# Optimization experiments

Hardware: AMD Instinct MI355X
Metric: run time of the kernel (lower is better)

Reference implementation:

```python
import jax, jax.numpy as jnp
import numpy as np

EPS = 1e-4  # ReEig eigenvalue clamp threshold (standard SPDNet value)


def _eig_apply(X, fn):
    # symmetric eig, apply fn to eigenvalues, reconstruct: V diag(fn(w)) V^T
    w, v = jnp.linalg.eigh(X)
    return jnp.einsum('...ij,...j,...kj->...ik', v, fn(w), v)


def _congr(P, G, mode):
    # CongrG: G^{+/-1/2} P G^{+/-1/2}, G is a single [n,n] SPD matrix
    w, v = jnp.linalg.eigh(G)
    s = jnp.sqrt(w) if mode == 'pos' else 1.0 / jnp.sqrt(w)
    Gs = (v * s) @ v.T  # [n,n]
    return Gs @ P @ Gs


def setup_inputs() -> dict:
    key = jax.random.key(0)
    ks = jax.random.split(key, 8)
    B, win, band, n, h, n_mid = 512, 3, 9, 22, 27, 32
    # SPD input covariance-like matrices
    M = jax.random.normal(ks[0], (B, win, band, n, n), dtype=jnp.float32)
    x = M @ jnp.swapaxes(M, -1, -2) / n + 0.5 * jnp.eye(n, dtype=jnp.float32)
    # Stiefel BiMap weights (orthonormal columns)
    W1, _ = jnp.linalg.qr(jax.random.normal(ks[1], (h, n_mid, n_mid), dtype=jnp.float32))
    Q2, _ = jnp.linalg.qr(jax.random.normal(ks[2], (h, n_mid, n_mid), dtype=jnp.float32))
    W2 = Q2[..., :n]
    running_mean = jnp.eye(n, dtype=jnp.float32)
    Aw = jax.random.normal(ks[3], (n, n), dtype=jnp.float32)
    bn_weight = Aw @ Aw.T / n + jnp.eye(n, dtype=jnp.float32)
    conv_w = jax.random.normal(ks[4], (48, 1, win, band * n * n), dtype=jnp.float32) * 0.01
    conv_b = jnp.zeros((48,), dtype=jnp.float32)
    fc_w = jax.random.normal(ks[5], (4, 48), dtype=jnp.float32) * 0.1
    fc_b = jnp.zeros((4,), dtype=jnp.float32)
    return {"x": x, "W1": W1, "W2": W2, "running_mean": running_mean,
            "bn_weight": bn_weight, "conv_w": conv_w, "conv_b": conv_b,
            "fc_w": fc_w, "fc_b": fc_b}


def reference(x, W1, W2, running_mean, bn_weight, conv_w, conv_b, fc_w, fc_b):
    B, win, band, n, _ = x.shape
    h = win * band
    no1 = W1.shape[-1]
    X = x.reshape(B, h, n, n)
    # SPDIncreaseDim(n -> no1): E X E^T + diag([0]*n + [1]*(no1-n))
    pad = no1 - n
    X = jnp.pad(X, ((0, 0), (0, 0), (0, pad), (0, pad)))
    X = X + jnp.diag(jnp.concatenate([jnp.zeros(n), jnp.ones(pad)])).astype(x.dtype)
    # BiMap 1 (per-channel W^T X W) + ReEig
    P = jnp.einsum('hni,bhnm,hmj->bhij', W1, X, W1)
    P = _eig_apply(P, lambda w: jnp.maximum(w, EPS))
    # BiMap 2
    P = jnp.einsum('hni,bhnm,hmj->bhij', W2, P, W2)
    # BatchNormSPD (eval mode): center by running_mean, scale by weight
    P = _congr(P, running_mean, 'neg')
    P = _congr(P, bn_weight, 'pos')
    # ReEig + LogEig
    P = _eig_apply(P, lambda w: jnp.maximum(w, EPS))
    P = _eig_apply(P, jnp.log)
    x_vec = P.reshape(B, win, band * n * n)
    feat = jnp.einsum('bhw,chw->bc', x_vec, conv_w[:, 0]) + conv_b  # [B, 48]
    return feat @ fc_w.T + fc_b                       # [B, classes]
```

## Files before the change

kernel.cpp:

```cpp
#include <hip/hip_runtime.h>


#define WS_CONST 484
#define WS_VT    512
#define WS_V     (512 + 13068)
#define WS_D     (13580 + 14256)
#define WS_G     (27836 + 13068)
#define G_STRIDE 528
#define V_STRIDE 528

typedef float v2f __attribute__((ext_vector_type(2)));

static __device__ __forceinline__ float dpp_shl1(float x) {
  return __int_as_float(__builtin_amdgcn_mov_dpp(__float_as_int(x), 0x101, 0xf, 0xf, true));
}
static __device__ __forceinline__ float upd_shr1(float old, float x) {
  return __int_as_float(__builtin_amdgcn_update_dpp(
      __float_as_int(old), __float_as_int(x), 0x111, 0xf, 0xf, false));
}

static __device__ __forceinline__ void rot_cs(float nL, float nR, float d,
                                              float& c, float& s,
                                              float& c2, float& ss, float& cs2) {
  float mu   = 0.5f*(nR - nL);
  float r2   = __builtin_fmaf(mu, mu, d*d);
  float invr = __builtin_amdgcn_rsqf(r2);
  bool  degen = (r2 < 1e-40f);
  float co = fminf(fabsf(mu)*invr, 1.0f);
  co = degen ? 1.0f : co;
  c2 = __builtin_fmaf(0.5f, co, 0.5f);
  c  = sqrtf(c2);
  float cinv = __builtin_amdgcn_rcpf(c);
  float t2 = d*invr;
  t2 = (mu < 0.0f) ? -t2 : t2;
  cs2 = degen ? 0.0f : t2;
  s  = 0.5f*cs2*cinv;
  ss = 1.0f - c2;
}

static __device__ __forceinline__ void jacobi_sweeps(v2f wl[11], v2f wr[11],
                                                     bool act, bool inert,
                                                     int minsweep, float eps2) {
  int okprev = 0;
  #pragma unroll 1
  for (int sweep = 0; sweep < 5; ++sweep) {
    if (sweep >= minsweep && __all(okprev)) break;
    v2f na = (v2f)(0.f), nb = (v2f)(0.f);
    #pragma unroll
    for (int i = 0; i < 11; ++i) { na += wl[i]*wl[i]; nb += wr[i]*wr[i]; }
    float nL = na.x + na.y, nR = nb.x + nb.y;
    float q = inert ? 0.f : (nL*nL + nR*nR);
    q += __shfl_xor(q, 1, 16);
    q += __shfl_xor(q, 2, 16);
    q += __shfl_xor(q, 4, 16);
    q += __shfl_xor(q, 8, 16);
    float dacc = 0.f;
    #pragma unroll 1
    for (int r = 0; r < 11; ++r) {
      {
        v2f da = (v2f)(0.f), db = (v2f)(0.f);
        #pragma unroll
        for (int i = 0; i < 10; i += 2) { da += wl[i]*wr[i]; db += wl[i+1]*wr[i+1]; }
        da += wl[10]*wr[10];
        float d = (da.x + da.y) + (db.x + db.y);
        dacc += d*d;
        float c, s, c2, ss, cs2;
        rot_cs(nL, nR, d, c, s, c2, ss, cs2);
        float nLn = c2*nL - cs2*d + ss*nR;
        float nRn = ss*nL + cs2*d + c2*nR;
        v2f cv = (v2f)(c), sv = (v2f)(s);
        #pragma unroll
        for (int i = 0; i < 11; ++i) {
          v2f nl = cv*wl[i] - sv*wr[i];
          v2f nr = sv*wl[i] + cv*wr[i];
          wl[i] = nr;
          wr[i] = nl;
        }
        nL = nRn; nR = nLn;
      }
      {
        v2f u[11];
        #pragma unroll
        for (int i = 0; i < 11; ++i) { u[i].x = dpp_shl1(wl[i].x); u[i].y = dpp_shl1(wl[i].y); }
        float nU = dpp_shl1(nL);
        v2f da = (v2f)(0.f), db = (v2f)(0.f);
        #pragma unroll
        for (int i = 0; i < 10; i += 2) { da += wr[i]*u[i]; db += wr[i+1]*u[i+1]; }
        da += wr[10]*u[10];
        float d = (da.x + da.y) + (db.x + db.y);
        d = act ? d : 0.f;
        dacc += d*d;
        float c, s, c2, ss, cs2;
        rot_cs(nR, nU, d, c, s, c2, ss, cs2);
        v2f cv = (v2f)(c), sv = (v2f)(s);
        #pragma unroll
        for (int i = 0; i < 11; ++i) {
          v2f rl = cv*wr[i] - sv*u[i];
          v2f rr = sv*wr[i] + cv*u[i];
          wr[i].x = act ? rr.x : wr[i].x;
          wr[i].y = act ? rr.y : wr[i].y;
          wl[i].x = upd_shr1(wl[i].x, rl.x);
          wl[i].y = upd_shr1(wl[i].y, rl.y);
        }
        float nRn = ss*nR + cs2*d + c2*nU;
        float nLg = c2*nR - cs2*d + ss*nU;
        nR = act ? nRn : nR;
        nL = upd_shr1(nL, nLg);
      }
    }
    float ds = inert ? 0.f : dacc;
    ds += __shfl_xor(ds, 1, 16);
    ds += __shfl_xor(ds, 2, 16);
    ds += __shfl_xor(ds, 4, 16);
    ds += __shfl_xor(ds, 8, 16);
    okprev = (ds <= eps2*q);
  }
}

__global__ void prep_kernel(const float* __restrict__ rm, const float* __restrict__ bn,
                            const float* __restrict__ W1, const float* __restrict__ W2,
                            const float* __restrict__ conv_w, const float* __restrict__ fc_w,
                            const float* __restrict__ conv_b, const float* __restrict__ fc_b,
                            float* __restrict__ ws, float* __restrict__ out) {
  __shared__ float sW1[1024] __attribute__((aligned(16)));
  __shared__ float sW2[704]  __attribute__((aligned(16)));
  __shared__ float sY[2][2][484] __attribute__((aligned(16)));
  __shared__ float sZ[2][2][484] __attribute__((aligned(16)));
  __shared__ float sT[2][484]    __attribute__((aligned(16)));
  __shared__ float sS[484]  __attribute__((aligned(16)));
  __shared__ float sU[704]  __attribute__((aligned(16)));
  __shared__ float sE[220]  __attribute__((aligned(16)));
  __shared__ float sG[1936] __attribute__((aligned(16)));
  __shared__ float sC[2];
  const int tid = threadIdx.x, h = blockIdx.x;

  if (h == 0)
    for (int idx = tid; idx < 2048; idx += 256) out[idx] = 0.f;

  const int wv = tid >> 6, ln = tid & 63;
  if (wv < 2) {
    const float* src = wv ? rm : bn;
    float s = 0.f;
    for (int i = ln; i < 484; i += 64) { float v = src[i]; s += v*v; }
    s += __shfl_xor(s, 1);  s += __shfl_xor(s, 2);  s += __shfl_xor(s, 4);
    s += __shfl_xor(s, 8);  s += __shfl_xor(s, 16); s += __shfl_xor(s, 32);
    if (ln == 0) sC[wv] = sqrtf(s);
  } else {
    const int t = tid - 128;
    for (int i = t; i < 1024; i += 128) sW1[i] = W1[h*1024 + i];
    for (int i = t; i < 704;  i += 128) sW2[i] = W2[h*704 + i];
  }
  __syncthreads();

  {
    const float ic0 = 1.0f/sC[0], ic1 = 1.0f/sC[1];
    for (int idx = tid; idx < 484; idx += 256) {
      const int i = idx/22, j = idx - 22*i;
      const float e = (i == j) ? 1.f : 0.f;
      sY[0][0][idx] = bn[idx]*ic0;  sZ[0][0][idx] = e;
      sY[1][0][idx] = rm[idx]*ic1;  sZ[1][0][idx] = e;
    }
  }
  __syncthreads();

  int cur = 0;
  #pragma unroll 1
  for (int it = 0; it < 11; ++it) {
    for (int idx = tid; idx < 484; idx += 256) {
      const int mt = (idx >= 242), r = idx - mt*242, i = r/11, jp = r - 11*i;
      const float* Zc = sZ[mt][cur];
      const float* Yc = sY[mt][cur];
      v2f acc = (v2f)(0.f);
      #pragma unroll
      for (int k = 0; k < 22; ++k)
        acc += *(const v2f*)(Yc + k*22 + 2*jp) * Zc[i*22 + k];
      v2f tv;
      tv.x = ((2*jp     == i) ? 3.f : 0.f) - acc.x;
      tv.y = ((2*jp + 1 == i) ? 3.f : 0.f) - acc.y;
      *(v2f*)(sT[mt] + i*22 + 2*jp) = tv;
    }
    __syncthreads();
    for (int idx = tid; idx < 968; idx += 256) {
      const int sel = idx/242, r = idx - 242*sel, i = r/11, jp = r - 11*i;
      const int mt = sel >> 1; const bool isZ = sel & 1;
      const float* A = isZ ? sT[mt] : sY[mt][cur];
      const float* B = isZ ? sZ[mt][cur] : sT[mt];
      v2f acc = (v2f)(0.f);
      #pragma unroll
      for (int k = 0; k < 22; ++k)
        acc += *(const v2f*)(B + k*22 + 2*jp) * A[i*22 + k];
      *(v2f*)((isZ ? sZ[mt][cur^1] : sY[mt][cur^1]) + i*22 + 2*jp) = 0.5f*acc;
    }
    __syncthreads();
    cur ^= 1;
  }

  {
    const float scale = sqrtf(sC[0]/sC[1]);
    const float* Zrm = sZ[1][cur];
    const float* Ybn = sY[0][cur];
    for (int idx = tid; idx < 484; idx += 256) {
      const int i = idx/22, j = idx - 22*i;
      float s = 0.f;
      for (int k = 0; k < 22; ++k) s += Zrm[i*22+k]*Ybn[k*22+j];
      sS[idx] = scale*s;
    }
  }
  for (int idx = tid; idx < 704; idx += 256) {
    const int n = idx/22, j = idx - 22*n;
    float s = 0.f;
    for (int k = 0; k < 32; ++k) s += sW1[n*32+k]*sW2[k*22+j];
    sU[idx] = s;
  }
  if (tid < 242) {
    const int wi = h/9, bi = h - 9*wi;
    const float* base = conv_w + wi*4356 + bi*484 + 2*tid;
    v2f a0 = (v2f)(0.f), a1 = (v2f)(0.f), a2 = (v2f)(0.f), a3 = (v2f)(0.f);
    #pragma unroll
    for (int c = 0; c < 48; ++c) {
      const v2f wv2 = *(const v2f*)(base + c*13068);
      a0 += wv2*fc_w[c];
      a1 += wv2*fc_w[48+c];
      a2 += wv2*fc_w[96+c];
      a3 += wv2*fc_w[144+c];
    }
    *(v2f*)(sG +        2*tid) = a0;
    *(v2f*)(sG +  484 + 2*tid) = a1;
    *(v2f*)(sG +  968 + 2*tid) = a2;
    *(v2f*)(sG + 1452 + 2*tid) = a3;
  }
  __syncthreads();

  for (int idx = tid; idx < 484; idx += 256) {
    const int k = idx/22, j = idx - 22*k;
    float s = 0.f;
    for (int l = 0; l < 22; ++l) s += sU[k*22+l]*sS[l*22+j];
    ws[WS_VT + h*484 + j*22 + k] = s;
    ws[WS_V  + h*V_STRIDE + k*24 + j] = s;
  }
  for (int idx = tid; idx < 220; idx += 256) {
    const int e = idx/22, j = idx - 22*e;
    float s = 0.f;
    for (int l = 0; l < 22; ++l) s += sU[(22+e)*22+l]*sS[l*22+j];
    sE[idx] = s;
  }
  __syncthreads();
  for (int idx = tid; idx < 484; idx += 256) {
    const int i = idx/22, j = idx - 22*i;
    float s = 0.f;
    for (int e = 0; e < 10; ++e) s += sE[e*22+i]*sE[e*22+j];
    ws[WS_D + h*484 + idx] = s;
  }
  for (int idx = tid; idx < 1936; idx += 256) {
    const int o = idx/484, r = idx - 484*o, i = r/22, j = r - 22*i;
    const float v = 0.5f*(sG[o*484 + i*22 + j] + sG[o*484 + j*22 + i]);
    const float gs = (j < i) ? 2.0f*v : ((j == i) ? v : 0.0f);
    ws[WS_G + (o*27+h)*G_STRIDE + i*24 + j] = gs;
  }
  if (h == 0 && tid < 4) {
    float s = 0.f;
    for (int c = 0; c < 48; ++c) s += fc_w[tid*48+c]*conv_b[c];
    ws[WS_CONST + tid] = s + fc_b[tid];
  }
}

__global__ void __launch_bounds__(64, 3) main_kernel(const float* __restrict__ x,
                                                     const float* __restrict__ ws,
                                                     float* __restrict__ out) {
  const int lane = threadIdx.x;
  const int g = lane >> 4, m = lane & 15;
  const int mm = (m < 10) ? m : 10;
  const int h  = blockIdx.x % 27;
  const int b  = (blockIdx.x/27)*4 + g;
  const int id = b*27 + h;

  v2f vl[11], vrr[11];
  {
    const v2f* vb = (const v2f*)(ws + WS_VT + h*484 + mm*44);
    #pragma unroll
    for (int j = 0; j < 11; ++j) { vl[j] = vb[j]; vrr[j] = vb[11+j]; }
  }
  v2f wl[11], wr[11];
  {
    const v2f* d2 = (const v2f*)(ws + WS_D + h*484 + mm*44);
    #pragma unroll
    for (int j = 0; j < 11; ++j) { wl[j] = d2[j]; wr[j] = d2[11+j]; }
  }
  {
    const v2f* X2 = (const v2f*)(x + (size_t)id * 484);
    const float* Vrow = ws + WS_V + h*V_STRIDE;
    #pragma unroll 2
    for (int k = 0; k < 22; ++k) {
      v2f aL = (v2f)(0.f), aR = (v2f)(0.f);
      #pragma unroll
      for (int c = 0; c < 11; ++c) {
        v2f xv = X2[11*k + c];
        aL += xv*vl[c];
        aR += xv*vrr[c];
      }
      float tLk = aL.x + aL.y, tRk = aR.x + aR.y;
      const v2f* vk = (const v2f*)(Vrow + k*24);
      #pragma unroll
      for (int j = 0; j < 11; ++j) {
        v2f q = vk[j];
        wl[j] += q*tLk;
        wr[j] += q*tRk;
      }
    }
  }

  jacobi_sweeps(wl, wr, (m < 10), (m > 10), 2, 1e-4f);

  float nL, nR;
  {
    v2f na = (v2f)(0.f), nb = (v2f)(0.f);
    #pragma unroll
    for (int i = 0; i < 11; ++i) { na += wl[i]*wl[i]; nb += wr[i]*wr[i]; }
    nL = na.x + na.y; nR = nb.x + nb.y;
  }
  const float HALF_LN2 = 0.34657359f;
  float coefL = HALF_LN2*log2f(fmaxf(nL, 1e-8f))*__builtin_amdgcn_rcpf(nL);
  float coefR = HALF_LN2*log2f(fmaxf(nR, 1e-8f))*__builtin_amdgcn_rcpf(nR);

  #pragma unroll 1
  for (int o = 0; o < 4; ++o) {
    const float* Gptr = ws + WS_G + (o*27+h)*G_STRIDE;
    float qL = 0.f, qR = 0.f;
    #pragma unroll
    for (int k = 0; k < 22; ++k) {
      const v2f* g2 = (const v2f*)(Gptr + k*24);
      v2f sa = (v2f)(0.f), ra = (v2f)(0.f);
      #pragma unroll
      for (int j = 0; j <= (k>>1); ++j) {
        v2f q = g2[j];
        sa += q*wl[j];
        ra += q*wr[j];
      }
      float wLk = wl[k>>1][k&1], wRk = wr[k>>1][k&1];
      qL += wLk*(sa.x + sa.y);
      qR += wRk*(ra.x + ra.y);
    }
    float v = (m <= 10) ? (coefL*qL + coefR*qR) : 0.0f;
    v += __shfl_down(v, 8, 16);
    v += __shfl_down(v, 4, 16);
    v += __shfl_down(v, 2, 16);
    v += __shfl_down(v, 1, 16);
    if (m == 0) {
      if (h == 0) v += ws[WS_CONST + o];
      atomicAdd(out + b*4 + o, v);
    }
  }
}

extern "C" void kernel_launch(void* const* d_in, const int* in_sizes, int n_in,
                              void* d_out, int out_size, void* d_ws, size_t ws_size,
                              hipStream_t stream) {
  const float* x   = (const float*)d_in[0];
  const float* W1  = (const float*)d_in[1];
  const float* W2  = (const float*)d_in[2];
  const float* rm  = (const float*)d_in[3];
  const float* bn  = (const float*)d_in[4];
  const float* cw  = (const float*)d_in[5];
  const float* cb  = (const float*)d_in[6];
  const float* fw  = (const float*)d_in[7];
  const float* fb  = (const float*)d_in[8];
  float* out = (float*)d_out;
  float* ws  = (float*)d_ws;

  prep_kernel<<<27, 256, 0, stream>>>(rm, bn, W1, W2, cw, fw, cb, fb, ws, out);
  main_kernel<<<3456, 64, 0, stream>>>(x, ws, out);
}
```

Before: 260.2 us.

## Process two independent matrices per lane group to interleave Jacobi sweeps

Each 16-lane group now carries two matrices (from batches b and b+4) through the projection, the Jacobi eigen-sweeps and the final quadratic-form reduction, with the two instruction streams interleaved. The grid is halved to 1728 blocks and launch bounds drop to 2 waves per SIMD to make room for the doubled register state. The goal is more instruction-level parallelism to hide the latency of the serial rotation chain and the DPP/shuffle operations. The costs are higher register pressure, lower occupancy, and joint sweep termination: a pair keeps iterating until both matrices converge.

Result: no change. 260.2 us (-0.0%).

```diff
diff --git a/kernel.cpp b/kernel.cpp
--- a/kernel.cpp
+++ b/kernel.cpp
@@ -38,82 +38,107 @@
   ss = 1.0f - c2;
 }
 
-static __device__ __forceinline__ void jacobi_sweeps(v2f wl[11], v2f wr[11],
-                                                     bool act, bool inert,
-                                                     int minsweep, float eps2) {
+static __device__ __forceinline__ void jacobi_sweeps2(v2f wl1[11], v2f wr1[11],
+                                                      v2f wl2[11], v2f wr2[11],
+                                                      bool act, bool inert,
+                                                      int minsweep, float eps2) {
   int okprev = 0;
   #pragma unroll 1
   for (int sweep = 0; sweep < 5; ++sweep) {
     if (sweep >= minsweep && __all(okprev)) break;
-    v2f na = (v2f)(0.f), nb = (v2f)(0.f);
-    #pragma unroll
-    for (int i = 0; i < 11; ++i) { na += wl[i]*wl[i]; nb += wr[i]*wr[i]; }
-    float nL = na.x + na.y, nR = nb.x + nb.y;
-    float q = inert ? 0.f : (nL*nL + nR*nR);
-    q += __shfl_xor(q, 1, 16);
-    q += __shfl_xor(q, 2, 16);
-    q += __shfl_xor(q, 4, 16);
-    q += __shfl_xor(q, 8, 16);
-    float dacc = 0.f;
+    v2f na1 = (v2f)(0.f), nb1 = (v2f)(0.f), na2 = (v2f)(0.f), nb2 = (v2f)(0.f);
+    #pragma unroll
+    for (int i = 0; i < 11; ++i) {
+      na1 += wl1[i]*wl1[i]; nb1 += wr1[i]*wr1[i];
+      na2 += wl2[i]*wl2[i]; nb2 += wr2[i]*wr2[i];
+    }
+    float nL1 = na1.x + na1.y, nR1 = nb1.x + nb1.y;
+    float nL2 = na2.x + na2.y, nR2 = nb2.x + nb2.y;
+    float q1 = inert ? 0.f : (nL1*nL1 + nR1*nR1);
+    float q2 = inert ? 0.f : (nL2*nL2 + nR2*nR2);
+    q1 += __shfl_xor(q1, 1, 16);  q2 += __shfl_xor(q2, 1, 16);
+    q1 += __shfl_xor(q1, 2, 16);  q2 += __shfl_xor(q2, 2, 16);
+    q1 += __shfl_xor(q1, 4, 16);  q2 += __shfl_xor(q2, 4, 16);
+    q1 += __shfl_xor(q1, 8, 16);  q2 += __shfl_xor(q2, 8, 16);
+    float dacc1 = 0.f, dacc2 = 0.f;
     #pragma unroll 1
     for (int r = 0; r < 11; ++r) {
       {
-        v2f da = (v2f)(0.f), db = (v2f)(0.f);
+        v2f da1 = (v2f)(0.f), da2 = (v2f)(0.f);
         #pragma unroll
-        for (int i = 0; i < 10; i += 2) { da += wl[i]*wr[i]; db += wl[i+1]*wr[i+1]; }
-        da += wl[10]*wr[10];
-        float d = (da.x + da.y) + (db.x + db.y);
-        dacc += d*d;
-        float c, s, c2, ss, cs2;
-        rot_cs(nL, nR, d, c, s, c2, ss, cs2);
-        float nLn = c2*nL - cs2*d + ss*nR;
-        float nRn = ss*nL + cs2*d + c2*nR;
-        v2f cv = (v2f)(c), sv = (v2f)(s);
+        for (int i = 0; i < 11; ++i) { da1 += wl1[i]*wr1[i]; da2 += wl2[i]*wr2[i]; }
+        float d1 = da1.x + da1.y, d2v = da2.x + da2.y;
+        dacc1 += d1*d1; dacc2 += d2v*d2v;
+        float c1, s1, c21, ss1, cs21; rot_cs(nL1, nR1, d1,  c1, s1, c21, ss1, cs21);
+        float c2_, s2_, c22, ss2, cs22; rot_cs(nL2, nR2, d2v, c2_, s2_, c22, ss2, cs22);
+        float nLn1 = c21*nL1 - cs21*d1 + ss1*nR1;
+        float nRn1 = ss1*nL1 + cs21*d1 + c21*nR1;
+        float nLn2 = c22*nL2 - cs22*d2v + ss2*nR2;
+        float nRn2 = ss2*nL2 + cs22*d2v + c22*nR2;
+        v2f cv1 = (v2f)(c1), sv1 = (v2f)(s1);
+        v2f cv2 = (v2f)(c2_), sv2 = (v2f)(s2_);
         #pragma unroll
         for (int i = 0; i < 11; ++i) {
-          v2f nl = cv*wl[i] - sv*wr[i];
-          v2f nr = sv*wl[i] + cv*wr[i];
-          wl[i] = nr;
-          wr[i] = nl;
+          v2f nl1 = cv1*wl1[i] - sv1*wr1[i];
+          v2f nr1 = sv1*wl1[i] + cv1*wr1[i];
+          wl1[i] = nr1; wr1[i] = nl1;
+          v2f nl2 = cv2*wl2[i] - sv2*wr2[i];
+          v2f nr2 = sv2*wl2[i] + cv2*wr2[i];
+          wl2[i] = nr2; wr2[i] = nl2;
         }
-        nL = nRn; nR = nLn;
+        nL1 = nRn1; nR1 = nLn1;
+        nL2 = nRn2; nR2 = nLn2;
       }
       {
-        v2f u[11];
-        #pragma unroll
-        for (int i = 0; i < 11; ++i) { u[i].x = dpp_shl1(wl[i].x); u[i].y = dpp_shl1(wl[i].y); }
-        float nU = dpp_shl1(nL);
-        v2f da = (v2f)(0.f), db = (v2f)(0.f);
-        #pragma unroll
-        for (int i = 0; i < 10; i += 2) { da += wr[i]*u[i]; db += wr[i+1]*u[i+1]; }
-        da += wr[10]*u[10];
-        float d = (da.x + da.y) + (db.x + db.y);
-        d = act ? d : 0.f;
-        dacc += d*d;
-        float c, s, c2, ss, cs2;
-        rot_cs(nR, nU, d, c, s, c2, ss, cs2);
-        v2f cv = (v2f)(c), sv = (v2f)(s);
+        v2f u1[11], u2[11];
         #pragma unroll
         for (int i = 0; i < 11; ++i) {
-          v2f rl = cv*wr[i] - sv*u[i];
-          v2f rr = sv*wr[i] + cv*u[i];
-          wr[i].x = act ? rr.x : wr[i].x;
-          wr[i].y = act ? rr.y : wr[i].y;
-          wl[i].x = upd_shr1(wl[i].x, rl.x);
-          wl[i].y = upd_shr1(wl[i].y, rl.y);
+          u1[i].x = dpp_shl1(wl1[i].x); u1[i].y = dpp_shl1(wl1[i].y);
+          u2[i].x = dpp_shl1(wl2[i].x); u2[i].y = dpp_shl1(wl2[i].y);
         }
-        float nRn = ss*nR + cs2*d + c2*nU;
-        float nLg = c2*nR - cs2*d + ss*nU;
-        nR = act ? nRn : nR;
-        nL = upd_shr1(nL, nLg);
+        float nU1 = dpp_shl1(nL1), nU2 = dpp_shl1(nL2);
+        v2f da1 = (v2f)(0.f), da2 = (v2f)(0.f);
+        #pragma unroll
+        for (int i = 0; i < 11; ++i) { da1 += wr1[i]*u1[i]; da2 += wr2[i]*u2[i]; }
+        float d1 = da1.x + da1.y, d2v = da2.x + da2.y;
+        d1 = act ? d1 : 0.f;  d2v = act ? d2v : 0.f;
+        dacc1 += d1*d1; dacc2 += d2v*d2v;
+        float c1, s1, c21, ss1, cs21; rot_cs(nR1, nU1, d1,  c1, s1, c21, ss1, cs21);
+        float c2_, s2_, c22, ss2, cs22; rot_cs(nR2, nU2, d2v, c2_, s2_, c22, ss2, cs22);
+        v2f cv1 = (v2f)(c1), sv1 = (v2f)(s1);
+        v2f cv2 = (v2f)(c2_), sv2 = (v2f)(s2_);
+        #pragma unroll
+        for (int i = 0; i < 11; ++i) {
+          v2f rl1 = cv1*wr1[i] - sv1*u1[i];
+          v2f rr1 = sv1*wr1[i] + cv1*u1[i];
+          wr1[i].x = act ? rr1.x : wr1[i].x;
+          wr1[i].y = act ? rr1.y : wr1[i].y;
+          wl1[i].x = upd_shr1(wl1[i].x, rl1.x);
+          wl1[i].y = upd_shr1(wl1[i].y, rl1.y);
+          v2f rl2 = cv2*wr2[i] - sv2*u2[i];
+          v2f rr2 = sv2*wr2[i] + cv2*u2[i];
+          wr2[i].x = act ? rr2.x : wr2[i].x;
+          wr2[i].y = act ? rr2.y : wr2[i].y;
+          wl2[i].x = upd_shr1(wl2[i].x, rl2.x);
+          wl2[i].y = upd_shr1(wl2[i].y, rl2.y);
+        }
+        float nRn1 = ss1*nR1 + cs21*d1 + c21*nU1;
+        float nLg1 = c21*nR1 - cs21*d1 + ss1*nU1;
+        nR1 = act ? nRn1 : nR1;
+        nL1 = upd_shr1(nL1, nLg1);
+        float nRn2 = ss2*nR2 + cs22*d2v + c22*nU2;
+        float nLg2 = c22*nR2 - cs22*d2v + ss2*nU2;
+        nR2 = act ? nRn2 : nR2;
+        nL2 = upd_shr1(nL2, nLg2);
       }
     }
-    float ds = inert ? 0.f : dacc;
-    ds += __shfl_xor(ds, 1, 16);
-    ds += __shfl_xor(ds, 2, 16);
-    ds += __shfl_xor(ds, 4, 16);
-    ds += __shfl_xor(ds, 8, 16);
-    okprev = (ds <= eps2*q);
+    float ds1 = inert ? 0.f : dacc1;
+    float ds2 = inert ? 0.f : dacc2;
+    ds1 += __shfl_xor(ds1, 1, 16);  ds2 += __shfl_xor(ds2, 1, 16);
+    ds1 += __shfl_xor(ds1, 2, 16);  ds2 += __shfl_xor(ds2, 2, 16);
+    ds1 += __shfl_xor(ds1, 4, 16);  ds2 += __shfl_xor(ds2, 4, 16);
+    ds1 += __shfl_xor(ds1, 8, 16);  ds2 += __shfl_xor(ds2, 8, 16);
+    okprev = (ds1 <= eps2*q1) && (ds2 <= eps2*q2);
   }
 }
 
@@ -264,90 +289,104 @@
   }
 }
 
-__global__ void __launch_bounds__(64, 3) main_kernel(const float* __restrict__ x,
+__global__ void __launch_bounds__(64, 2) main_kernel(const float* __restrict__ x,
                                                      const float* __restrict__ ws,
                                                      float* __restrict__ out) {
   const int lane = threadIdx.x;
   const int g = lane >> 4, m = lane & 15;
   const int mm = (m < 10) ? m : 10;
   const int h  = blockIdx.x % 27;
-  const int b  = (blockIdx.x/27)*4 + g;
-  const int id = b*27 + h;
-
-  v2f vl[11], vrr[11];
-  {
-    const v2f* vb = (const v2f*)(ws + WS_VT + h*484 + mm*44);
-    #pragma unroll
-    for (int j = 0; j < 11; ++j) { vl[j] = vb[j]; vrr[j] = vb[11+j]; }
-  }
-  v2f wl[11], wr[11];
+  const int bb = (blockIdx.x/27)*8;
+  const int b1 = bb + g, b2 = bb + 4 + g;
+  const size_t id1 = (size_t)(b1*27 + h), id2 = (size_t)(b2*27 + h);
+
+  v2f wl1[11], wr1[11], wl2[11], wr2[11];
   {
     const v2f* d2 = (const v2f*)(ws + WS_D + h*484 + mm*44);
     #pragma unroll
-    for (int j = 0; j < 11; ++j) { wl[j] = d2[j]; wr[j] = d2[11+j]; }
+    for (int j = 0; j < 11; ++j) {
+      v2f a = d2[j], bvv = d2[11+j];
+      wl1[j] = a; wl2[j] = a;
+      wr1[j] = bvv; wr2[j] = bvv;
+    }
   }
   {
-    const v2f* X2 = (const v2f*)(x + (size_t)id * 484);
+    v2f vl[11], vrr[11];
+    const v2f* vb = (const v2f*)(ws + WS_VT + h*484 + mm*44);
+    #pragma unroll
+    for (int j = 0; j < 11; ++j) { vl[j] = vb[j]; vrr[j] = vb[11+j]; }
+    const v2f* Xa = (const v2f*)(x + id1 * 484);
+    const v2f* Xb = (const v2f*)(x + id2 * 484);
     const float* Vrow = ws + WS_V + h*V_STRIDE;
     #pragma unroll 2
     for (int k = 0; k < 22; ++k) {
-      v2f aL = (v2f)(0.f), aR = (v2f)(0.f);
+      v2f aL1 = (v2f)(0.f), aR1 = (v2f)(0.f), aL2 = (v2f)(0.f), aR2 = (v2f)(0.f);
       #pragma unroll
       for (int c = 0; c < 11; ++c) {
-        v2f xv = X2[11*k + c];
-        aL += xv*vl[c];
-        aR += xv*vrr[c];
+        v2f xv1 = Xa[11*k + c], xv2 = Xb[11*k + c];
+        aL1 += xv1*vl[c];  aR1 += xv1*vrr[c];
+        aL2 += xv2*vl[c];  aR2 += xv2*vrr[c];
       }
-      float tLk = aL.x + aL.y, tRk = aR.x + aR.y;
+      float tL1 = aL1.x + aL1.y, tR1 = aR1.x + aR1.y;
+      float tL2 = aL2.x + aL2.y, tR2 = aR2.x + aR2.y;
       const v2f* vk = (const v2f*)(Vrow + k*24);
       #pragma unroll
       for (int j = 0; j < 11; ++j) {
         v2f q = vk[j];
-        wl[j] += q*tLk;
-        wr[j] += q*tRk;
+        wl1[j] += q*tL1;  wr1[j] += q*tR1;
+        wl2[j] += q*tL2;  wr2[j] += q*tR2;
       }
     }
   }
 
-  jacobi_sweeps(wl, wr, (m < 10), (m > 10), 2, 1e-4f);
-
-  float nL, nR;
+  jacobi_sweeps2(wl1, wr1, wl2, wr2, (m < 10), (m > 10), 2, 1e-4f);
+
+  float nL1, nR1, nL2, nR2;
   {
-    v2f na = (v2f)(0.f), nb = (v2f)(0.f);
-    #pragma unroll
-    for (int i = 0; i < 11; ++i) { na += wl[i]*wl[i]; nb += wr[i]*wr[i]; }
-    nL = na.x + na.y; nR = nb.x + nb.y;
+    v2f a1 = (v2f)(0.f), bq1 = (v2f)(0.f), a2 = (v2f)(0.f), bq2 = (v2f)(0.f);
+    #pragma unroll
+    for (int i = 0; i < 11; ++i) {
+      a1 += wl1[i]*wl1[i]; bq1 += wr1[i]*wr1[i];
+      a2 += wl2[i]*wl2[i]; bq2 += wr2[i]*wr2[i];
+    }
+    nL1 = a1.x + a1.y; nR1 = bq1.x + bq1.y;
+    nL2 = a2.x + a2.y; nR2 = bq2.x + bq2.y;
   }
   const float HALF_LN2 = 0.34657359f;
-  float coefL = HALF_LN2*log2f(fmaxf(nL, 1e-8f))*__builtin_amdgcn_rcpf(nL);
-  float coefR = HALF_LN2*log2f(fmaxf(nR, 1e-8f))*__builtin_amdgcn_rcpf(nR);
+  float coefL1 = HALF_LN2*log2f(fmaxf(nL1, 1e-8f))*__builtin_amdgcn_rcpf(nL1);
+  float coefR1 = HALF_LN2*log2f(fmaxf(nR1, 1e-8f))*__builtin_amdgcn_rcpf(nR1);
+  float coefL2 = HALF_LN2*log2f(fmaxf(nL2, 1e-8f))*__builtin_amdgcn_rcpf(nL2);
+  float coefR2 = HALF_LN2*log2f(fmaxf(nR2, 1e-8f))*__builtin_amdgcn_rcpf(nR2);
 
   #pragma unroll 1
   for (int o = 0; o < 4; ++o) {
     const float* Gptr = ws + WS_G + (o*27+h)*G_STRIDE;
-    float qL = 0.f, qR = 0.f;
+    float qL1 = 0.f, qR1 = 0.f, qL2 = 0.f, qR2 = 0.f;
     #pragma unroll
     for (int k = 0; k < 22; ++k) {
       const v2f* g2 = (const v2f*)(Gptr + k*24);
-      v2f sa = (v2f)(0.f), ra = (v2f)(0.f);
+      v2f sa1 = (v2f)(0.f), ra1 = (v2f)(0.f), sa2 = (v2f)(0.f), ra2 = (v2f)(0.f);
       #pragma unroll
       for (int j = 0; j <= (k>>1); ++j) {
         v2f q = g2[j];
-        sa += q*wl[j];
-        ra += q*wr[j];
+        sa1 += q*wl1[j];  ra1 += q*wr1[j];
+        sa2 += q*wl2[j];  ra2 += q*wr2[j];
       }
-      float wLk = wl[k>>1][k&1], wRk = wr[k>>1][k&1];
-      qL += wLk*(sa.x + sa.y);
-      qR += wRk*(ra.x + ra.y);
-    }
-    float v = (m <= 10) ? (coefL*qL + coefR*qR) : 0.0f;
-    v += __shfl_down(v, 8, 16);
-    v += __shfl_down(v, 4, 16);
-    v += __shfl_down(v, 2, 16);
-    v += __shfl_down(v, 1, 16);
+      float wL1 = wl1[k>>1][k&1], wR1 = wr1[k>>1][k&1];
+      float wL2 = wl2[k>>1][k&1], wR2 = wr2[k>>1][k&1];
+      qL1 += wL1*(sa1.x + sa1.y);  qR1 += wR1*(ra1.x + ra1.y);
+      qL2 += wL2*(sa2.x + sa2.y);  qR2 += wR2*(ra2.x + ra2.y);
+    }
+    float v1 = (m <= 10) ? (coefL1*qL1 + coefR1*qR1) : 0.0f;
+    float v2 = (m <= 10) ? (coefL2*qL2 + coefR2*qR2) : 0.0f;
+    v1 += __shfl_down(v1, 8, 16);  v2 += __shfl_down(v2, 8, 16);
+    v1 += __shfl_down(v1, 4, 16);  v2 += __shfl_down(v2, 4, 16);
+    v1 += __shfl_down(v1, 2, 16);  v2 += __shfl_down(v2, 2, 16);
+    v1 += __shfl_down(v1, 1, 16);  v2 += __shfl_down(v2, 1, 16);
     if (m == 0) {
-      if (h == 0) v += ws[WS_CONST + o];
-      atomicAdd(out + b*4 + o, v);
+      if (h == 0) { v1 += ws[WS_CONST + o]; v2 += ws[WS_CONST + o]; }
+      atomicAdd(out + b1*4 + o, v1);
+      atomicAdd(out + b2*4 + o, v2);
     }
   }
 }
@@ -368,5 +407,5 @@
   float* ws  = (float*)d_ws;
 
   prep_kernel<<<27, 256, 0, stream>>>(rm, bn, W1, W2, cw, fw, cb, fb, ws, out);
-  main_kernel<<<3456, 64, 0, stream>>>(x, ws, out);
-}
+  main_kernel<<<1728, 64, 0, stream>>>(x, ws, out);
+}
```
